# Kernel optimization log

Measured on AMD Instinct MI355X. Metric: run time of the kernel, lower is better.

## Reference

```python
import jax, jax.numpy as jnp
import numpy as np

EPS = 1e-5
ND, NDIS, NP, NG, NPW = 40000, 40000, 80000, 80000, 40000
D = 128


def gcn(x_src, src, dst, n_dst, W, b):
    # DGL GraphConv with norm='both': D_dst^{-1/2} A^T D_src^{-1/2} X W + b
    deg_out = jnp.maximum(jnp.zeros((x_src.shape[0],), x_src.dtype).at[src].add(1.0), 1.0)
    xs = x_src * (deg_out ** -0.5)[:, None]
    msg = jax.ops.segment_sum(xs[src], dst, num_segments=n_dst)
    deg_in = jnp.maximum(jnp.zeros((n_dst,), x_src.dtype).at[dst].add(1.0), 1.0)
    return (msg * (deg_in ** -0.5)[:, None]) @ W + b


def bn_prelu(v, gamma, beta, a):
    # BatchNorm1d (training-mode batch stats, biased var) then PReLU (scalar slope)
    mu = v.mean(0)
    var = v.var(0)
    y = gamma * (v - mu) / jnp.sqrt(var + EPS) + beta
    return jnp.where(y >= 0, y, a * y)


def sem_att(z, W1, b1, w2):
    # z: [N, K, D]; shared SemanticAttention across node types
    s = jnp.tanh(z @ W1 + b1) @ w2        # [N, K]
    beta = jax.nn.softmax(s.mean(0))       # [K]
    return jnp.einsum('k,nkd->nd', beta, z)


def setup_inputs():
    key = jax.random.key(0)
    ks = iter(jax.random.split(key, 40))
    f = lambda n: jax.random.normal(next(ks), (n, D), jnp.float32)
    inp = {'h_drug': f(ND), 'h_disease': f(NDIS), 'h_protein': f(NP),
           'h_gene': f(NG), 'h_pathway': f(NPW)}
    rels = {'dd': (ND, ND, 640000), 'ddi': (ND, NDIS, 640000), 'disdis': (NDIS, NDIS, 640000),
            'dp': (ND, NP, 640000), 'pp': (NP, NP, 1280000), 'pg': (NP, NG, 1280000),
            'gg': (NG, NG, 1280000), 'gpw': (NG, NPW, 1280000), 'pwpw': (NPW, NPW, 640000),
            'pwdis': (NPW, NDIS, 640000)}
    for name, (ns, nd, E) in rels.items():
        inp[name + '_src'] = jax.random.randint(next(ks), (E,), 0, ns)
        inp[name + '_dst'] = jax.random.randint(next(ks), (E,), 0, nd)
    inp['W_blocks'] = jax.random.normal(next(ks), (5, 3, D, D), jnp.float32) * 0.09
    inp['b_blocks'] = jnp.zeros((5, 3, D), jnp.float32)
    inp['bn_gamma'] = jnp.ones((5, D), jnp.float32)
    inp['bn_beta'] = jnp.zeros((5, D), jnp.float32)
    inp['prelu_a'] = jnp.full((5,), 0.25, jnp.float32)
    inp['attn_W1'] = jax.random.normal(next(ks), (D, D), jnp.float32) * 0.09
    inp['attn_b1'] = jnp.zeros((D,), jnp.float32)
    inp['attn_w2'] = jax.random.normal(next(ks), (D,), jnp.float32) * 0.09
    return inp


def reference(h_drug, h_disease, h_protein, h_gene, h_pathway,
              dd_src, dd_dst, ddi_src, ddi_dst, disdis_src, disdis_dst,
              dp_src, dp_dst, pp_src, pp_dst, pg_src, pg_dst,
              gg_src, gg_dst, gpw_src, gpw_dst, pwpw_src, pwpw_dst,
              pwdis_src, pwdis_dst,
              W_blocks, b_blocks, bn_gamma, bn_beta, prelu_a,
              attn_W1, attn_b1, attn_w2):
    act = lambda i, v: bn_prelu(v, bn_gamma[i], bn_beta[i], prelu_a[i])
    # block 0: drug_disease  (rels: drug_drug, drug_disease, disease_disease)
    d0 = act(0, gcn(h_drug, dd_src, dd_dst, ND, W_blocks[0, 0], b_blocks[0, 0]))
    dis0 = act(0, gcn(h_drug, ddi_src, ddi_dst, NDIS, W_blocks[0, 1], b_blocks[0, 1])
               + gcn(h_disease, disdis_src, disdis_dst, NDIS, W_blocks[0, 2], b_blocks[0, 2]))
    # block 1: drug_protein
    d1 = act(1, gcn(h_drug, dd_src, dd_dst, ND, W_blocks[1, 0], b_blocks[1, 0]))
    p1 = act(1, gcn(h_drug, dp_src, dp_dst, NP, W_blocks[1, 1], b_blocks[1, 1])
             + gcn(h_protein, pp_src, pp_dst, NP, W_blocks[1, 2], b_blocks[1, 2]))
    # block 2: protein_gene
    p2 = act(2, gcn(h_protein, pp_src, pp_dst, NP, W_blocks[2, 0], b_blocks[2, 0]))
    g2 = act(2, gcn(h_protein, pg_src, pg_dst, NG, W_blocks[2, 1], b_blocks[2, 1])
             + gcn(h_gene, gg_src, gg_dst, NG, W_blocks[2, 2], b_blocks[2, 2]))
    # block 3: gene_pathway
    g3 = act(3, gcn(h_gene, gg_src, gg_dst, NG, W_blocks[3, 0], b_blocks[3, 0]))
    pw3 = act(3, gcn(h_gene, gpw_src, gpw_dst, NPW, W_blocks[3, 1], b_blocks[3, 1])
              + gcn(h_pathway, pwpw_src, pwpw_dst, NPW, W_blocks[3, 2], b_blocks[3, 2]))
    # block 4: pathway_disease
    pw4 = act(4, gcn(h_pathway, pwpw_src, pwpw_dst, NPW, W_blocks[4, 0], b_blocks[4, 0]))
    dis4 = act(4, gcn(h_pathway, pwdis_src, pwdis_dst, NDIS, W_blocks[4, 1], b_blocks[4, 1])
               + gcn(h_disease, disdis_src, disdis_dst, NDIS, W_blocks[4, 2], b_blocks[4, 2]))
    att = lambda a, b: sem_att(jnp.stack([a, b], axis=1), attn_W1, attn_b1, attn_w2)
    return (att(d0, d1), att(dis0, dis4), att(p1, p2), att(g2, g3), att(pw3, pw4))
```

## Files before the change

kernel.cpp:

```cpp
#include <hip/hip_runtime.h>
#include <hip/hip_bf16.h>

#define D128 128

typedef __attribute__((ext_vector_type(8))) short bf16x8;
typedef __attribute__((ext_vector_type(4))) float f32x4;

__device__ inline unsigned short f2bf(float f) {
    unsigned u = __float_as_uint(f);
    u = u + 0x7fffu + ((u >> 16) & 1u);
    return (unsigned short)(u >> 16);
}
__device__ inline float bf2f(unsigned short h) {
    return __uint_as_float(((unsigned)h) << 16);
}
__device__ inline float fast_tanh(float x) {
    float e = __expf(2.f * x);
    return 1.f - 2.f * __builtin_amdgcn_rcpf(e + 1.f);
}

__device__ __forceinline__ void stage_w(const unsigned short* __restrict__ Wt,
                                        unsigned short* lw, int t)
{
    const uint4* srcW = (const uint4*)Wt;
    uint4* dstW = (uint4*)lw;
    for (int i = t; i < 2048; i += 256) {
        int row = i >> 4, sl = i & 15;
        dstW[row * 16 + (sl ^ (row & 7))] = srcW[i];
    }
}
__device__ __forceinline__ bf16x8 read_w(const unsigned short* lw, int row, int kt, int lq)
{
    int slot = (kt * 4 + lq) ^ (row & 7);
    return *(const bf16x8*)(lw + row * 128 + slot * 8);
}

__global__ __launch_bounds__(256) void xconv(const float* __restrict__ in,
                                             unsigned* __restrict__ out, int n_u)
{
    int i = blockIdx.x * 256 + threadIdx.x;
    if (i * 4 >= n_u) return;
    const float4* in4 = (const float4*)(in + (size_t)i * 8);
    float4 a = in4[0], b = in4[1];
    uint4 o;
    o.x = (unsigned)f2bf(a.x) | ((unsigned)f2bf(a.y) << 16);
    o.y = (unsigned)f2bf(a.z) | ((unsigned)f2bf(a.w) << 16);
    o.z = (unsigned)f2bf(b.x) | ((unsigned)f2bf(b.y) << 16);
    o.w = (unsigned)f2bf(b.z) | ((unsigned)f2bf(b.w) << 16);
    ((uint4*)out)[i] = o;
}

__global__ void wconv_t(const float* __restrict__ W_blocks, const float* __restrict__ W1,
                        unsigned short* __restrict__ wt)
{
    int m = blockIdx.x;
    const float* src = (m < 15) ? (W_blocks + (size_t)m * 16384) : W1;
    unsigned short* dst = wt + (size_t)m * 16384;
    for (int i = threadIdx.x; i < 16384; i += 256) {
        int n = i >> 7, k = i & 127;
        dst[i] = f2bf(src[k * 128 + n]);
    }
}

struct BuildArgs {
    const int* esrc[10]; const int* edst[10];
    int* histD; int* histS;
    int cumBlk[11]; int dstColBase[11]; int srcColBase[11]; int E[10];
};

__global__ __launch_bounds__(256) void part_count(BuildArgs A)
{
    __shared__ int hd[640], hs[640];
    int blk = blockIdx.x, t = threadIdx.x;
    int r = 0;
    while (r < 9 && blk >= A.cumBlk[r + 1]) r++;
    int blkInRel = blk - A.cumBlk[r];
    int nbD = A.dstColBase[r + 1] - A.dstColBase[r];
    int nbS = A.srcColBase[r + 1] - A.srcColBase[r];
    for (int i = t; i < nbD; i += 256) hd[i] = 0;
    for (int i = t; i < nbS; i += 256) hs[i] = 0;
    __syncthreads();
    int e0 = blkInRel * 4096;
    const int* sp = A.esrc[r];
    const int* dp = A.edst[r];
    int E = A.E[r];
#pragma unroll
    for (int j = 0; j < 16; j++) {
        int e = e0 + j * 256 + t;
        if (e < E) {
            atomicAdd(&hd[dp[e] >> 7], 1);
            atomicAdd(&hs[sp[e] >> 7], 1);
        }
    }
    __syncthreads();
    int cd = A.dstColBase[r], cs = A.srcColBase[r];
    for (int i = t; i < nbD; i += 256)
        A.histD[(size_t)(cd + i) * 313 + blkInRel] = hd[i];
    for (int i = t; i < nbS; i += 256)
        A.histS[(size_t)(cs + i) * 313 + blkInRel] = hs[i];
}

struct ScanArgs { int* hist; int* totals; int colBase[11]; int cumBlk[11]; };

__global__ __launch_bounds__(256) void col_scan(ScanArgs A)
{
    __shared__ int v[320];
    int col = blockIdx.x, t = threadIdx.x;
    int r = 0;
    while (r < 9 && col >= A.colBase[r + 1]) r++;
    int nblk = A.cumBlk[r + 1] - A.cumBlk[r];
    for (int i = t; i < nblk; i += 256) v[i] = A.hist[(size_t)col * 313 + i];
    __syncthreads();
    if (t == 0) {
        int run = 0;
        for (int i = 0; i < nblk; i++) { int c = v[i]; v[i] = run; run += c; }
        A.totals[col] = run;
    }
    __syncthreads();
    for (int i = t; i < nblk; i += 256) A.hist[(size_t)col * 313 + i] = v[i];
}

__global__ __launch_bounds__(256) void base_scan(const int* __restrict__ totals,
                                                 int* __restrict__ colbase, int n)
{
    __shared__ int v[4384];
    int t = threadIdx.x;
    for (int i = t; i < n; i += 256) v[i] = totals[i];
    __syncthreads();
    if (t == 0) {
        int run = 0;
        for (int i = 0; i < n; i++) { int c = v[i]; v[i] = run; run += c; }
        v[n] = run;
    }
    __syncthreads();
    for (int i = t; i <= n; i += 256) colbase[i] = v[i];
}

struct ScatArgs {
    const int* esrc[10]; const int* edst[10];
    const int* hist; const int* colbase; int* epart;
    int cumBlk[11]; int colBase[11]; int E[10];
};

__global__ __launch_bounds__(256) void part_scatter(ScatArgs A)
{
    __shared__ int h[640];
    __shared__ int base[640];
    int blk = blockIdx.x, t = threadIdx.x;
    int r = 0;
    while (r < 9 && blk >= A.cumBlk[r + 1]) r++;
    int blkInRel = blk - A.cumBlk[r];
    int colb = A.colBase[r];
    int nb = A.colBase[r + 1] - colb;
    for (int i = t; i < nb; i += 256) {
        base[i] = A.colbase[colb + i] + A.hist[(size_t)(colb + i) * 313 + blkInRel];
        h[i] = 0;
    }
    __syncthreads();
    int e0 = blkInRel * 4096;
    const int* sp = A.esrc[r];
    const int* dp = A.edst[r];
    int E = A.E[r];
#pragma unroll
    for (int j = 0; j < 16; j++) {
        int e = e0 + j * 256 + t;
        if (e < E) {
            int d = dp[e];
            int b = d >> 7;
            int p = atomicAdd(&h[b], 1);
            A.epart[base[b] + p] = (sp[e] & 0x1FFFF) | ((d & 127) << 17);
        }
    }
}

struct SScatArgs {
    const int* esrc[10];
    const int* hist; const int* colbase; unsigned char* spart;
    int cumBlk[11]; int colBase[11]; int E[10];
};

__global__ __launch_bounds__(256) void scatter_src(SScatArgs A)
{
    __shared__ int h[640];
    __shared__ int base[640];
    int blk = blockIdx.x, t = threadIdx.x;
    int r = 0;
    while (r < 9 && blk >= A.cumBlk[r + 1]) r++;
    int blkInRel = blk - A.cumBlk[r];
    int colb = A.colBase[r];
    int nb = A.colBase[r + 1] - colb;
    for (int i = t; i < nb; i += 256) {
        base[i] = A.colbase[colb + i] + A.hist[(size_t)(colb + i) * 313 + blkInRel];
        h[i] = 0;
    }
    __syncthreads();
    int e0 = blkInRel * 4096;
    const int* sp = A.esrc[r];
    int E = A.E[r];
#pragma unroll
    for (int j = 0; j < 16; j++) {
        int e = e0 + j * 256 + t;
        if (e < E) {
            int s = sp[e];
            int b = s >> 7;
            int p = atomicAdd(&h[b], 1);
            A.spart[(size_t)base[b] + p] = (unsigned char)(s & 127);
        }
    }
}

struct FillArgs {
    const int* epart; const int* colbase;
    int* cursor; int* ebuf; int* oflow;
    int colBase[11];
    int cursorBase[10]; int ebufBase[10]; int cap[10]; int nd[10];
};

__global__ __launch_bounds__(256) void bucket_fill(FillArgs A)
{
    __shared__ int lcur[128];
    int col = blockIdx.x, t = threadIdx.x;
    int r = 0;
    while (r < 9 && col >= A.colBase[r + 1]) r++;
    int b = col - A.colBase[r];
    if (t < 128) lcur[t] = 0;
    __syncthreads();
    int start = A.colbase[col], end = A.colbase[col + 1];
    int cap = A.cap[r];
    int* eb = A.ebuf + (size_t)A.ebufBase[r];
    int* ofl = A.oflow + r * 8194;
    for (int i = start + t; i < end; i += 256) {
        int v = A.epart[i];
        int s = v & 0x1FFFF;
        int dlow = (v >> 17) & 127;
        int p = atomicAdd(&lcur[dlow], 1);
        if (p < cap) eb[(size_t)(b * 128 + dlow) * cap + p] = s;
        else {
            int q = atomicAdd(&ofl[0], 1);
            if (q < 4095) { ofl[2 + 2 * q] = b * 128 + dlow; ofl[3 + 2 * q] = s; }
        }
    }
    __syncthreads();
    if (t < 128) {
        int d = b * 128 + t;
        if (d < A.nd[r]) A.cursor[A.cursorBase[r] + d] = lcur[t];
    }
}

struct DegArgs {
    const unsigned char* spart; const int* colbase;
    int* degs;
    int colBase[11]; int degsBase[10]; int ns[10];
};

__global__ __launch_bounds__(256) void deg_count(DegArgs A)
{
    __shared__ int lc[128];
    int col = blockIdx.x, t = threadIdx.x;
    int r = 0;
    while (r < 9 && col >= A.colBase[r + 1]) r++;
    int b = col - A.colBase[r];
    if (t < 128) lc[t] = 0;
    __syncthreads();
    int start = A.colbase[col], end = A.colbase[col + 1];
    for (int i = start + t; i < end; i += 256)
        atomicAdd(&lc[A.spart[i]], 1);
    __syncthreads();
    if (t < 128) {
        int s = b * 128 + t;
        if (s < A.ns[r]) A.degs[A.degsBase[r] + s] = lc[t];
    }
}

__global__ __launch_bounds__(256) void gather_bf16(
    const unsigned* __restrict__ Xb, const int* __restrict__ degs,
    const int* __restrict__ cursor, const int* __restrict__ ebuf,
    const int* __restrict__ oflow, unsigned* __restrict__ aggb, int nd, int cap)
{
    int t = threadIdx.x;
    int lane = t & 63, r = t >> 6;
    int d = blockIdx.x * 4 + r;
    if (d >= nd) return;
    int cnt = cursor[d];
    int end = min(cnt, cap);
    const int* eb = ebuf + (size_t)d * cap;
    float a0 = 0.f, a1 = 0.f;
    int i = 0;
    for (; i + 4 <= end; i += 4) {
        int s0 = eb[i], s1 = eb[i + 1], s2 = eb[i + 2], s3 = eb[i + 3];
        float c0 = rsqrtf((float)max(degs[s0], 1));
        float c1 = rsqrtf((float)max(degs[s1], 1));
        float c2 = rsqrtf((float)max(degs[s2], 1));
        float c3 = rsqrtf((float)max(degs[s3], 1));
        unsigned x0 = Xb[(size_t)s0 * 64 + lane];
        unsigned x1 = Xb[(size_t)s1 * 64 + lane];
        unsigned x2 = Xb[(size_t)s2 * 64 + lane];
        unsigned x3 = Xb[(size_t)s3 * 64 + lane];
        a0 = fmaf(bf2f((unsigned short)(x0 & 0xffff)), c0, a0);
        a1 = fmaf(bf2f((unsigned short)(x0 >> 16)), c0, a1);
        a0 = fmaf(bf2f((unsigned short)(x1 & 0xffff)), c1, a0);
        a1 = fmaf(bf2f((unsigned short)(x1 >> 16)), c1, a1);
        a0 = fmaf(bf2f((unsigned short)(x2 & 0xffff)), c2, a0);
        a1 = fmaf(bf2f((unsigned short)(x2 >> 16)), c2, a1);
        a0 = fmaf(bf2f((unsigned short)(x3 & 0xffff)), c3, a0);
        a1 = fmaf(bf2f((unsigned short)(x3 >> 16)), c3, a1);
    }
    for (; i < end; i++) {
        int s0 = eb[i];
        float c0 = rsqrtf((float)max(degs[s0], 1));
        unsigned x0 = Xb[(size_t)s0 * 64 + lane];
        a0 = fmaf(bf2f((unsigned short)(x0 & 0xffff)), c0, a0);
        a1 = fmaf(bf2f((unsigned short)(x0 >> 16)), c0, a1);
    }
    if (cnt > cap) {
        int n = min(oflow[0], 4095);
        for (int ii = 0; ii < n; ii++) {
            if (oflow[2 + 2 * ii] == d) {
                int s0 = oflow[3 + 2 * ii];
                float c0 = rsqrtf((float)max(degs[s0], 1));
                unsigned x0 = Xb[(size_t)s0 * 64 + lane];
                a0 = fmaf(bf2f((unsigned short)(x0 & 0xffff)), c0, a0);
                a1 = fmaf(bf2f((unsigned short)(x0 >> 16)), c0, a1);
            }
        }
    }
    float sc = rsqrtf((float)max(cnt, 1));
    a0 *= sc; a1 *= sc;
    aggb[(size_t)d * 64 + lane] = (unsigned)f2bf(a0) | ((unsigned)f2bf(a1) << 16);
}

__device__ __forceinline__ void epi_store(
    f32x4* acc, unsigned short* __restrict__ Vb, int accum, int do_stats,
    float* ssum, float* ssq, int row0, int lr, int lq)
{
#pragma unroll
    for (int n = 0; n < 8; n++) {
        int col = n * 16 + lr;
        float s_ = 0.f, q_ = 0.f;
#pragma unroll
        for (int reg = 0; reg < 4; reg++) {
            int row = row0 + lq * 4 + reg;
            float v = acc[n][reg];
            unsigned short* vp = &Vb[(size_t)row * D128 + col];
            if (accum) v += bf2f(*vp);
            *vp = f2bf(v);
            s_ += v; q_ += v * v;
        }
        if (do_stats) {
            s_ += __shfl_xor(s_, 16); s_ += __shfl_xor(s_, 32);
            q_ += __shfl_xor(q_, 16); q_ += __shfl_xor(q_, 32);
            if (lq == 0) {
                atomicAdd(&ssum[col], s_);
                atomicAdd(&ssq[col], q_);
            }
        }
    }
}

__global__ __launch_bounds__(256) void gemm_mfma(
    const unsigned short* __restrict__ A, const unsigned short* __restrict__ Wt,
    unsigned short* __restrict__ Vb, int accum, int do_stats, float* __restrict__ statsraw)
{
    __shared__ unsigned short lw[16384];
    __shared__ float ssum[128], ssq[128];
    int t = threadIdx.x;
    int wave = t >> 6, lane = t & 63;
    int lr = lane & 15, lq = lane >> 4;
    int row0 = blockIdx.x * 64 + wave * 16;

    if (t < 128) { ssum[t] = 0.f; ssq[t] = 0.f; }
    stage_w(Wt, lw, t);
    __syncthreads();

    f32x4 acc[8];
#pragma unroll
    for (int n = 0; n < 8; n++) acc[n] = (f32x4)(0.f);

    const unsigned short* arow = A + (size_t)(row0 + lr) * 128 + lq * 8;
#pragma unroll
    for (int kt = 0; kt < 4; kt++) {
        bf16x8 af = *(const bf16x8*)(arow + kt * 32);
#pragma unroll
        for (int n = 0; n < 8; n++) {
            bf16x8 bfr = read_w(lw, n * 16 + lr, kt, lq);
            acc[n] = __builtin_amdgcn_mfma_f32_16x16x32_bf16(af, bfr, acc[n], 0, 0, 0);
        }
    }
    epi_store(acc, Vb, accum, do_stats, ssum, ssq, row0, lr, lq);
    if (do_stats) {
        __syncthreads();
        if (t < 128) atomicAdd(&statsraw[t], ssum[t]);
        else atomicAdd(&statsraw[t], ssq[t - 128]);
    }
}

__global__ __launch_bounds__(256) void gemm_mfma2(
    const unsigned short* __restrict__ A,
    const unsigned short* __restrict__ Wt0, const unsigned short* __restrict__ Wt1,
    unsigned short* __restrict__ V0b, unsigned short* __restrict__ V1b,
    int acc0f, int acc1f, int st0, int st1,
    float* __restrict__ sr0, float* __restrict__ sr1)
{
    __shared__ unsigned short lw0[16384], lw1[16384];
    __shared__ float ssum0[128], ssq0[128], ssum1[128], ssq1[128];
    int t = threadIdx.x;
    int wave = t >> 6, lane = t & 63;
    int lr = lane & 15, lq = lane >> 4;
    int row0 = blockIdx.x * 64 + wave * 16;

    if (t < 128) { ssum0[t] = 0.f; ssq0[t] = 0.f; ssum1[t] = 0.f; ssq1[t] = 0.f; }
    stage_w(Wt0, lw0, t);
    stage_w(Wt1, lw1, t);
    __syncthreads();

    f32x4 acc0[8], acc1[8];
#pragma unroll
    for (int n = 0; n < 8; n++) { acc0[n] = (f32x4)(0.f); acc1[n] = (f32x4)(0.f); }

    const unsigned short* arow = A + (size_t)(row0 + lr) * 128 + lq * 8;
#pragma unroll
    for (int kt = 0; kt < 4; kt++) {
        bf16x8 af = *(const bf16x8*)(arow + kt * 32);
#pragma unroll
        for (int n = 0; n < 8; n++) {
            int row = n * 16 + lr;
            bf16x8 b0 = read_w(lw0, row, kt, lq);
            bf16x8 b1 = read_w(lw1, row, kt, lq);
            acc0[n] = __builtin_amdgcn_mfma_f32_16x16x32_bf16(af, b0, acc0[n], 0, 0, 0);
            acc1[n] = __builtin_amdgcn_mfma_f32_16x16x32_bf16(af, b1, acc1[n], 0, 0, 0);
        }
    }
    epi_store(acc0, V0b, acc0f, st0, ssum0, ssq0, row0, lr, lq);
    epi_store(acc1, V1b, acc1f, st1, ssum1, ssq1, row0, lr, lq);
    __syncthreads();
    if (st0) {
        if (t < 128) atomicAdd(&sr0[t], ssum0[t]);
        else atomicAdd(&sr0[t], ssq0[t - 128]);
    }
    if (st1) {
        if (t < 128) atomicAdd(&sr1[t], ssum1[t]);
        else atomicAdd(&sr1[t], ssq1[t - 128]);
    }
}

struct FinArgs { int Ms[10]; };

__global__ void bn_finalize(const float* __restrict__ raw, float* __restrict__ fin, FinArgs fa)
{
    int tt = blockIdx.x;
    int c = threadIdx.x;
    float m = (float)fa.Ms[tt];
    float s = raw[tt * 256 + c], sq = raw[tt * 256 + 128 + c];
    float mu = s / m;
    float var = fmaxf(sq / m - mu * mu, 0.f);
    fin[tt * 256 + c] = mu;
    fin[tt * 256 + 128 + c] = rsqrtf(var + 1e-5f);
}

__global__ __launch_bounds__(256) void attn_t(
    const unsigned short* __restrict__ Vb, const float* __restrict__ raw, float Minv,
    const float* __restrict__ gam, const float* __restrict__ bet,
    const float* __restrict__ pa,
    const unsigned short* __restrict__ W1t, const float* __restrict__ b1,
    const float* __restrict__ w2, float* __restrict__ Sout)
{
    __shared__ float st[256];
    __shared__ float red[4];
    int t = threadIdx.x;
    if (t < 128) {
        float mu = raw[t] * Minv;
        float var = fmaxf(raw[128 + t] * Minv - mu * mu, 0.f);
        st[t] = mu;
        st[128 + t] = rsqrtf(var + 1e-5f);
    }
    __syncthreads();

    int wave = t >> 6, lane = t & 63;
    int lr = lane & 15, lq = lane >> 4;
    int row0 = blockIdx.x * 64 + wave * 16;
    float a = *pa;

    f32x4 acc[8];
#pragma unroll
    for (int n = 0; n < 8; n++) acc[n] = (f32x4)(0.f);

    const unsigned short* vrow = Vb + (size_t)(row0 + lr) * D128;
#pragma unroll
    for (int kt = 0; kt < 4; kt++) {
        int k0 = kt * 32 + lq * 8;
        bf16x8 vv = *(const bf16x8*)(vrow + k0);
        bf16x8 af;
#pragma unroll
        for (int jj = 0; jj < 8; jj++) {
            int cc = k0 + jj;
            float y = bf2f((unsigned short)vv[jj]);
            float yy = gam[cc] * (y - st[cc]) * st[128 + cc] + bet[cc];
            yy = yy >= 0.f ? yy : a * yy;
            af[jj] = (short)f2bf(yy);
        }
#pragma unroll
        for (int n = 0; n < 8; n++) {
            bf16x8 bfr = *(const bf16x8*)(W1t + (size_t)(n * 16 + lr) * 128 + k0);
            acc[n] = __builtin_amdgcn_mfma_f32_16x16x32_bf16(af, bfr, acc[n], 0, 0, 0);
        }
    }

    float thr = 0.f;
#pragma unroll
    for (int n = 0; n < 8; n++) {
        int col = n * 16 + lr;
        float bc = b1[col], wc = w2[col];
#pragma unroll
        for (int reg = 0; reg < 4; reg++)
            thr += fast_tanh(acc[n][reg] + bc) * wc;
    }
#pragma unroll
    for (int off = 1; off < 64; off <<= 1)
        thr += __shfl_xor(thr, off);
    if (lane == 0) red[wave] = thr;
    __syncthreads();
    if (t == 0) atomicAdd(Sout, red[0] + red[1] + red[2] + red[3]);
}

struct CombArgs {
    float* outp[5]; const unsigned short* va[5]; const unsigned short* vb[5];
    const float* stats; const float* gam; const float* bet; const float* pa; const float* S;
    int ta[5]; int tb[5]; int blka[5]; int blkb[5]; float invM[5]; int cum[6];
};

__global__ void combine_all(CombArgs D)
{
    int b = blockIdx.x, t = threadIdx.x;
    int p = 0;
    while (p < 4 && b >= D.cum[p + 1]) p++;
    size_t idx = (size_t)(b - D.cum[p]) * 256 + t;
    int c = (int)(idx & 127);
    float s0 = D.S[2 * p] * D.invM[p], s1 = D.S[2 * p + 1] * D.invM[p];
    float mx = fmaxf(s0, s1);
    float e0 = expf(s0 - mx), e1 = expf(s1 - mx);
    float inv = 1.f / (e0 + e1);
    float b0 = e0 * inv, b1w = e1 * inv;
    const float* sta = D.stats + D.ta[p] * 256;
    const float* stb = D.stats + D.tb[p] * 256;
    const float* ga = D.gam + D.blka[p] * 128;
    const float* ba = D.bet + D.blka[p] * 128;
    const float* gb = D.gam + D.blkb[p] * 128;
    const float* bb = D.bet + D.blkb[p] * 128;
    float aa = D.pa[D.blka[p]], ab = D.pa[D.blkb[p]];
    float va = bf2f(D.va[p][idx]);
    float vb = bf2f(D.vb[p][idx]);
    float ya = ga[c] * (va - sta[c]) * sta[128 + c] + ba[c];
    ya = ya >= 0.f ? ya : aa * ya;
    float yb = gb[c] * (vb - stb[c]) * stb[128 + c] + bb[c];
    yb = yb >= 0.f ? yb : ab * yb;
    D.outp[p][idx] = b0 * ya + b1w * yb;
}

extern "C" void kernel_launch(void* const* d_in, const int* in_sizes, int n_in,
                              void* d_out, int out_size, void* d_ws, size_t ws_size,
                              hipStream_t stream)
{
    const float* feats[5] = {
        (const float*)d_in[0], (const float*)d_in[1], (const float*)d_in[2],
        (const float*)d_in[3], (const float*)d_in[4]
    };
    const int featN[5] = {40000, 40000, 80000, 80000, 40000};
    const float* W_blocks = (const float*)d_in[25];
    const float* bn_gamma = (const float*)d_in[27];
    const float* bn_beta  = (const float*)d_in[28];
    const float* prelu_a  = (const float*)d_in[29];
    const float* attn_W1  = (const float*)d_in[30];
    const float* attn_b1  = (const float*)d_in[31];
    const float* attn_w2  = (const float*)d_in[32];
    float* out = (float*)d_out;

    unsigned* xbf  = (unsigned*)out;
    unsigned* aggb = (unsigned*)(out + 5120000);
    int*      ebuf = (int*)(out + 10240000);

    float* wsf = (float*)d_ws;
    unsigned short* wsvb = (unsigned short*)wsf;
    unsigned short* wtbf = (unsigned short*)(wsf + 35840000);
    int* degs     = (int*)(wsf + 35971072);
    int* cursor   = degs + 560000;
    int* oflow    = cursor + 560000;
    int* histD    = oflow + 81940;
    int* histS    = histD + 1370314;
    int* colbaseD = histS + 1370314;
    int* totalsD  = colbaseD + 4379;
    int* colbaseS = totalsD + 4378;
    int* totalsS  = colbaseS + 4379;
    int* epart    = totalsS + 4378;
    unsigned char* spart = (unsigned char*)(epart + 8960000);
    float* statsraw = (float*)(epart + 8960000 + 2240000);
    float* statsfin = statsraw + 2560;
    float* Ssum     = statsfin + 2560;
    size_t needed = ((size_t)((float*)(Ssum + 16) - wsf)) * 4;
    if (ws_size < needed) return;

    const int Mt[10]  = {40000, 40000, 40000, 40000, 80000, 80000, 80000, 80000, 40000, 40000};
    const int blk[10] = {0, 1, 0, 4, 1, 2, 2, 3, 3, 4};
    size_t offV[10];
    {
        size_t o = 0;
        for (int t = 0; t < 10; t++) { offV[t] = o; o += (size_t)Mt[t] * 128; }
    }
    unsigned short* Vb[10];
    for (int t = 0; t < 10; t++) Vb[t] = wsvb + offV[t];
    const size_t offT[5] = {0, 5120000, 10240000, 20480000, 30720000};

    const int relFeat[10] = {0, 0, 0, 1, 2, 2, 3, 3, 4, 4};
    const int relSrc[10]  = {5, 7, 11, 9, 13, 15, 17, 19, 21, 23};
    const int relNs[10]   = {40000, 40000, 40000, 40000, 80000, 80000, 80000, 80000, 40000, 40000};
    const int relNd[10]   = {40000, 40000, 80000, 40000, 80000, 80000, 80000, 40000, 40000, 40000};
    const int relE[10]    = {640000, 640000, 640000, 640000, 1280000,
                             1280000, 1280000, 1280000, 640000, 640000};
    const int relCap[10]  = {40, 40, 24, 40, 40, 40, 40, 56, 40, 40};
    const int cumBlk[11]  = {0, 157, 314, 471, 628, 941, 1254, 1567, 1880, 2037, 2194};
    const int dstColBase[11] = {0, 313, 626, 1251, 1564, 2189, 2814, 3439, 3752, 4065, 4378};
    const int srcColBase[11] = {0, 313, 626, 939, 1252, 1877, 2502, 3127, 3752, 4065, 4378};
    const int degsBase[10]   = {0, 40000, 80000, 120000, 160000, 240000, 320000, 400000, 480000, 520000};
    const int cursorBase[10] = {0, 40000, 80000, 160000, 200000, 280000, 360000, 440000, 480000, 520000};
    const int ebufBase[10]   = {0, 1600000, 3200000, 5120000, 6720000, 9920000,
                                13120000, 16320000, 18560000, 20160000};

    struct GJob { int tid; int widx; int accum; int stats; };
    const int relNjob[10] = {2, 1, 1, 2, 2, 1, 2, 1, 2, 1};
    const GJob relJob[10][2] = {
        {{0,  0, 0, 1}, {1,  3, 0, 1}},
        {{2,  1, 0, 0}, {0,  0, 0, 0}},
        {{4,  4, 0, 0}, {0,  0, 0, 0}},
        {{2,  2, 1, 1}, {3, 14, 0, 0}},
        {{4,  5, 1, 1}, {5,  6, 0, 1}},
        {{6,  7, 0, 0}, {0,  0, 0, 0}},
        {{6,  8, 1, 1}, {7,  9, 0, 1}},
        {{8, 10, 0, 0}, {0,  0, 0, 0}},
        {{8, 11, 1, 1}, {9, 12, 0, 1}},
        {{3, 13, 1, 1}, {0,  0, 0, 0}},
    };
    const int doneCnt[10] = {2, 0, 0, 1, 2, 0, 2, 0, 2, 1};
    const int doneT[10][2] = {{0,1},{0,0},{0,0},{2,0},{4,5},{0,0},{6,7},{0,0},{8,9},{3,0}};

    wconv_t<<<16, 256, 0, stream>>>(W_blocks, attn_W1, wtbf);
    hipMemsetAsync(statsraw, 0, (2560 + 2560 + 16) * sizeof(float), stream);
    hipMemsetAsync(oflow, 0, (size_t)81940 * sizeof(int), stream);

    BuildArgs BA;
    ScanArgs  SAD, SAS;
    ScatArgs  CA;
    SScatArgs SSA;
    FillArgs  FA;
    DegArgs   DA;
    for (int r = 0; r < 10; r++) {
        BA.esrc[r] = (const int*)d_in[relSrc[r]];
        BA.edst[r] = (const int*)d_in[relSrc[r] + 1];
        BA.E[r] = relE[r];
        CA.esrc[r] = BA.esrc[r]; CA.edst[r] = BA.edst[r]; CA.E[r] = relE[r];
        SSA.esrc[r] = BA.esrc[r]; SSA.E[r] = relE[r];
        FA.cursorBase[r] = cursorBase[r];
        FA.ebufBase[r] = ebufBase[r];
        FA.cap[r] = relCap[r];
        FA.nd[r] = relNd[r];
        DA.degsBase[r] = degsBase[r];
        DA.ns[r] = relNs[r];
    }
    for (int i = 0; i < 11; i++) {
        BA.cumBlk[i] = cumBlk[i]; BA.dstColBase[i] = dstColBase[i]; BA.srcColBase[i] = srcColBase[i];
        SAD.colBase[i] = dstColBase[i]; SAD.cumBlk[i] = cumBlk[i];
        SAS.colBase[i] = srcColBase[i]; SAS.cumBlk[i] = cumBlk[i];
        CA.cumBlk[i] = cumBlk[i]; CA.colBase[i] = dstColBase[i];
        SSA.cumBlk[i] = cumBlk[i]; SSA.colBase[i] = srcColBase[i];
        FA.colBase[i] = dstColBase[i];
        DA.colBase[i] = srcColBase[i];
    }
    BA.histD = histD; BA.histS = histS;
    SAD.hist = histD; SAD.totals = totalsD;
    SAS.hist = histS; SAS.totals = totalsS;
    CA.hist = histD; CA.colbase = colbaseD; CA.epart = epart;
    SSA.hist = histS; SSA.colbase = colbaseS; SSA.spart = spart;
    FA.epart = epart; FA.colbase = colbaseD;
    FA.cursor = cursor; FA.ebuf = ebuf; FA.oflow = oflow;
    DA.spart = spart; DA.colbase = colbaseS; DA.degs = degs;

    part_count<<<2194, 256, 0, stream>>>(BA);
    col_scan<<<4378, 256, 0, stream>>>(SAD);
    col_scan<<<4378, 256, 0, stream>>>(SAS);
    base_scan<<<1, 256, 0, stream>>>(totalsD, colbaseD, 4378);
    base_scan<<<1, 256, 0, stream>>>(totalsS, colbaseS, 4378);
    part_scatter<<<2194, 256, 0, stream>>>(CA);
    scatter_src<<<2194, 256, 0, stream>>>(SSA);
    bucket_fill<<<4378, 256, 0, stream>>>(FA);
    deg_count<<<4378, 256, 0, stream>>>(DA);

    int lastFeat = -1;
    for (int r = 0; r < 10; r++) {
        if (relFeat[r] != lastFeat) {
            lastFeat = relFeat[r];
            int n_u = featN[lastFeat] * 64;
            xconv<<<(n_u / 4 + 255) / 256, 256, 0, stream>>>(feats[lastFeat], xbf, n_u);
        }
        gather_bf16<<<relNd[r] / 4, 256, 0, stream>>>(
            xbf, degs + degsBase[r], cursor + cursorBase[r],
            ebuf + (size_t)ebufBase[r], oflow + r * 8194, aggb, relNd[r], relCap[r]);
        if (relNjob[r] == 2) {
            const GJob& G0 = relJob[r][0];
            const GJob& G1 = relJob[r][1];
            gemm_mfma2<<<relNd[r] / 64, 256, 0, stream>>>(
                (const unsigned short*)aggb,
                wtbf + (size_t)G0.widx * 16384, wtbf + (size_t)G1.widx * 16384,
                Vb[G0.tid], Vb[G1.tid], G0.accum, G1.accum, G0.stats, G1.stats,
                statsraw + (size_t)G0.tid * 256, statsraw + (size_t)G1.tid * 256);
        } else {
            const GJob& G = relJob[r][0];
            gemm_mfma<<<relNd[r] / 64, 256, 0, stream>>>(
                (const unsigned short*)aggb, wtbf + (size_t)G.widx * 16384,
                Vb[G.tid], G.accum, G.stats, statsraw + (size_t)G.tid * 256);
        }
        for (int k = 0; k < doneCnt[r]; k++) {
            int t = doneT[r][k];
            attn_t<<<Mt[t] / 64, 256, 0, stream>>>(
                Vb[t], statsraw + (size_t)t * 256, 1.0f / Mt[t],
                bn_gamma + blk[t] * 128, bn_beta + blk[t] * 128, prelu_a + blk[t],
                wtbf + (size_t)15 * 16384, attn_b1, attn_w2, Ssum + t);
        }
    }

    FinArgs fa;
    for (int t = 0; t < 10; t++) fa.Ms[t] = Mt[t];
    bn_finalize<<<10, 128, 0, stream>>>(statsraw, statsfin, fa);

    CombArgs CD;
    CD.stats = statsfin; CD.gam = bn_gamma; CD.bet = bn_beta; CD.pa = prelu_a; CD.S = Ssum;
    CD.cum[0] = 0;
    for (int p = 0; p < 5; p++) {
        CD.outp[p] = out + offT[p];
        CD.va[p] = Vb[p * 2];
        CD.vb[p] = Vb[p * 2 + 1];
        CD.ta[p] = p * 2; CD.tb[p] = p * 2 + 1;
        CD.blka[p] = blk[p * 2]; CD.blkb[p] = blk[p * 2 + 1];
        CD.invM[p] = 1.0f / Mt[p * 2];
        CD.cum[p + 1] = CD.cum[p] + Mt[p * 2] / 2;
    }
    combine_all<<<CD.cum[5], 256, 0, stream>>>(CD);
}
```

Before: 1.673 ms.

## Prescale source features by degree, widen partition buckets, fuse scatter kernels

The bf16 feature conversion now folds the source-degree rsqrt scale into the converted rows, so the gather no longer reads degs per edge or does a multiply per neighbour. Partition buckets grow from 128 to 512 destination rows and 256 source rows, which shrinks the histogram, scan and fill grids. The separate dst and src scatter passes are merged into one kernel that reads each edge once. In exchange, the conversion runs once per relation instead of once per feature change, and the larger buckets put more LDS atomic contention on each block.

Measured after the change: 1.617 ms. 1.03x faster.

```diff
diff --git a/kernel.cpp b/kernel.cpp
--- a/kernel.cpp
+++ b/kernel.cpp
@@ -35,19 +35,18 @@
     return *(const bf16x8*)(lw + row * 128 + slot * 8);
 }
 
-__global__ __launch_bounds__(256) void xconv(const float* __restrict__ in,
-                                             unsigned* __restrict__ out, int n_u)
-{
-    int i = blockIdx.x * 256 + threadIdx.x;
-    if (i * 4 >= n_u) return;
-    const float4* in4 = (const float4*)(in + (size_t)i * 8);
-    float4 a = in4[0], b = in4[1];
-    uint4 o;
-    o.x = (unsigned)f2bf(a.x) | ((unsigned)f2bf(a.y) << 16);
-    o.y = (unsigned)f2bf(a.z) | ((unsigned)f2bf(a.w) << 16);
-    o.z = (unsigned)f2bf(b.x) | ((unsigned)f2bf(b.y) << 16);
-    o.w = (unsigned)f2bf(b.z) | ((unsigned)f2bf(b.w) << 16);
-    ((uint4*)out)[i] = o;
+__global__ __launch_bounds__(256) void xconv_scaled(
+    const float* __restrict__ in, const int* __restrict__ degs,
+    unsigned* __restrict__ out, int nrows)
+{
+    int t = threadIdx.x;
+    int lane = t & 63, rr = t >> 6;
+    int row = blockIdx.x * 4 + rr;
+    if (row >= nrows) return;
+    float sc = rsqrtf((float)max(degs[row], 1));
+    float2 v = ((const float2*)(in + (size_t)row * 128))[lane];
+    out[(size_t)row * 64 + lane] =
+        (unsigned)f2bf(v.x * sc) | ((unsigned)f2bf(v.y * sc) << 16);
 }
 
 __global__ void wconv_t(const float* __restrict__ W_blocks, const float* __restrict__ W1,
@@ -70,7 +69,7 @@
 
 __global__ __launch_bounds__(256) void part_count(BuildArgs A)
 {
-    __shared__ int hd[640], hs[640];
+    __shared__ int hd[160], hs[320];
     int blk = blockIdx.x, t = threadIdx.x;
     int r = 0;
     while (r < 9 && blk >= A.cumBlk[r + 1]) r++;
@@ -88,8 +87,8 @@
     for (int j = 0; j < 16; j++) {
         int e = e0 + j * 256 + t;
         if (e < E) {
-            atomicAdd(&hd[dp[e] >> 7], 1);
-            atomicAdd(&hs[sp[e] >> 7], 1);
+            atomicAdd(&hd[dp[e] >> 9], 1);
+            atomicAdd(&hs[sp[e] >> 8], 1);
         }
     }
     __syncthreads();
@@ -123,7 +122,7 @@
 __global__ __launch_bounds__(256) void base_scan(const int* __restrict__ totals,
                                                  int* __restrict__ colbase, int n)
 {
-    __shared__ int v[4384];
+    __shared__ int v[2200];
     int t = threadIdx.x;
     for (int i = t; i < n; i += 256) v[i] = totals[i];
     __syncthreads();
@@ -138,23 +137,29 @@
 
 struct ScatArgs {
     const int* esrc[10]; const int* edst[10];
-    const int* hist; const int* colbase; int* epart;
-    int cumBlk[11]; int colBase[11]; int E[10];
+    const int* histD; const int* colbaseD;
+    const int* histS; const int* colbaseS;
+    int* epart; unsigned char* spart;
+    int cumBlk[11]; int dstColBase[11]; int srcColBase[11]; int E[10];
 };
 
-__global__ __launch_bounds__(256) void part_scatter(ScatArgs A)
-{
-    __shared__ int h[640];
-    __shared__ int base[640];
+__global__ __launch_bounds__(256) void scatter_all(ScatArgs A)
+{
+    __shared__ int hd[160], based[160], hs[320], bases[320];
     int blk = blockIdx.x, t = threadIdx.x;
     int r = 0;
     while (r < 9 && blk >= A.cumBlk[r + 1]) r++;
     int blkInRel = blk - A.cumBlk[r];
-    int colb = A.colBase[r];
-    int nb = A.colBase[r + 1] - colb;
-    for (int i = t; i < nb; i += 256) {
-        base[i] = A.colbase[colb + i] + A.hist[(size_t)(colb + i) * 313 + blkInRel];
-        h[i] = 0;
+    int cd = A.dstColBase[r], cs = A.srcColBase[r];
+    int nbD = A.dstColBase[r + 1] - cd;
+    int nbS = A.srcColBase[r + 1] - cs;
+    for (int i = t; i < nbD; i += 256) {
+        based[i] = A.colbaseD[cd + i] + A.histD[(size_t)(cd + i) * 313 + blkInRel];
+        hd[i] = 0;
+    }
+    for (int i = t; i < nbS; i += 256) {
+        bases[i] = A.colbaseS[cs + i] + A.histS[(size_t)(cs + i) * 313 + blkInRel];
+        hs[i] = 0;
     }
     __syncthreads();
     int e0 = blkInRel * 4096;
@@ -165,46 +170,13 @@
     for (int j = 0; j < 16; j++) {
         int e = e0 + j * 256 + t;
         if (e < E) {
-            int d = dp[e];
-            int b = d >> 7;
-            int p = atomicAdd(&h[b], 1);
-            A.epart[base[b] + p] = (sp[e] & 0x1FFFF) | ((d & 127) << 17);
-        }
-    }
-}
-
-struct SScatArgs {
-    const int* esrc[10];
-    const int* hist; const int* colbase; unsigned char* spart;
-    int cumBlk[11]; int colBase[11]; int E[10];
-};
-
-__global__ __launch_bounds__(256) void scatter_src(SScatArgs A)
-{
-    __shared__ int h[640];
-    __shared__ int base[640];
-    int blk = blockIdx.x, t = threadIdx.x;
-    int r = 0;
-    while (r < 9 && blk >= A.cumBlk[r + 1]) r++;
-    int blkInRel = blk - A.cumBlk[r];
-    int colb = A.colBase[r];
-    int nb = A.colBase[r + 1] - colb;
-    for (int i = t; i < nb; i += 256) {
-        base[i] = A.colbase[colb + i] + A.hist[(size_t)(colb + i) * 313 + blkInRel];
-        h[i] = 0;
-    }
-    __syncthreads();
-    int e0 = blkInRel * 4096;
-    const int* sp = A.esrc[r];
-    int E = A.E[r];
-#pragma unroll
-    for (int j = 0; j < 16; j++) {
-        int e = e0 + j * 256 + t;
-        if (e < E) {
-            int s = sp[e];
-            int b = s >> 7;
-            int p = atomicAdd(&h[b], 1);
-            A.spart[(size_t)base[b] + p] = (unsigned char)(s & 127);
+            int s = sp[e], d = dp[e];
+            int bd = d >> 9;
+            int pd = atomicAdd(&hd[bd], 1);
+            A.epart[based[bd] + pd] = (s & 0x1FFFF) | ((d & 511) << 17);
+            int bs = s >> 8;
+            int ps = atomicAdd(&hs[bs], 1);
+            A.spart[(size_t)bases[bs] + ps] = (unsigned char)(s & 255);
         }
     }
 }
@@ -218,12 +190,12 @@
 
 __global__ __launch_bounds__(256) void bucket_fill(FillArgs A)
 {
-    __shared__ int lcur[128];
+    __shared__ int lcur[512];
     int col = blockIdx.x, t = threadIdx.x;
     int r = 0;
     while (r < 9 && col >= A.colBase[r + 1]) r++;
     int b = col - A.colBase[r];
-    if (t < 128) lcur[t] = 0;
+    for (int i = t; i < 512; i += 256) lcur[i] = 0;
     __syncthreads();
     int start = A.colbase[col], end = A.colbase[col + 1];
     int cap = A.cap[r];
@@ -232,18 +204,18 @@
     for (int i = start + t; i < end; i += 256) {
         int v = A.epart[i];
         int s = v & 0x1FFFF;
-        int dlow = (v >> 17) & 127;
+        int dlow = (v >> 17) & 511;
         int p = atomicAdd(&lcur[dlow], 1);
-        if (p < cap) eb[(size_t)(b * 128 + dlow) * cap + p] = s;
+        if (p < cap) eb[(size_t)(b * 512 + dlow) * cap + p] = s;
         else {
             int q = atomicAdd(&ofl[0], 1);
-            if (q < 4095) { ofl[2 + 2 * q] = b * 128 + dlow; ofl[3 + 2 * q] = s; }
-        }
-    }
-    __syncthreads();
-    if (t < 128) {
-        int d = b * 128 + t;
-        if (d < A.nd[r]) A.cursor[A.cursorBase[r] + d] = lcur[t];
+            if (q < 4095) { ofl[2 + 2 * q] = b * 512 + dlow; ofl[3 + 2 * q] = s; }
+        }
+    }
+    __syncthreads();
+    for (int i = t; i < 512; i += 256) {
+        int d = b * 512 + i;
+        if (d < A.nd[r]) A.cursor[A.cursorBase[r] + d] = lcur[i];
     }
 }
 
@@ -255,25 +227,23 @@
 
 __global__ __launch_bounds__(256) void deg_count(DegArgs A)
 {
-    __shared__ int lc[128];
+    __shared__ int lc[256];
     int col = blockIdx.x, t = threadIdx.x;
     int r = 0;
     while (r < 9 && col >= A.colBase[r + 1]) r++;
     int b = col - A.colBase[r];
-    if (t < 128) lc[t] = 0;
+    lc[t] = 0;
     __syncthreads();
     int start = A.colbase[col], end = A.colbase[col + 1];
     for (int i = start + t; i < end; i += 256)
         atomicAdd(&lc[A.spart[i]], 1);
     __syncthreads();
-    if (t < 128) {
-        int s = b * 128 + t;
-        if (s < A.ns[r]) A.degs[A.degsBase[r] + s] = lc[t];
-    }
+    int s = b * 256 + t;
+    if (s < A.ns[r]) A.degs[A.degsBase[r] + s] = lc[t];
 }
 
 __global__ __launch_bounds__(256) void gather_bf16(
-    const unsigned* __restrict__ Xb, const int* __restrict__ degs,
+    const unsigned* __restrict__ Xb,
     const int* __restrict__ cursor, const int* __restrict__ ebuf,
     const int* __restrict__ oflow, unsigned* __restrict__ aggb, int nd, int cap)
 {
@@ -288,39 +258,29 @@
     int i = 0;
     for (; i + 4 <= end; i += 4) {
         int s0 = eb[i], s1 = eb[i + 1], s2 = eb[i + 2], s3 = eb[i + 3];
-        float c0 = rsqrtf((float)max(degs[s0], 1));
-        float c1 = rsqrtf((float)max(degs[s1], 1));
-        float c2 = rsqrtf((float)max(degs[s2], 1));
-        float c3 = rsqrtf((float)max(degs[s3], 1));
         unsigned x0 = Xb[(size_t)s0 * 64 + lane];
         unsigned x1 = Xb[(size_t)s1 * 64 + lane];
         unsigned x2 = Xb[(size_t)s2 * 64 + lane];
         unsigned x3 = Xb[(size_t)s3 * 64 + lane];
-        a0 = fmaf(bf2f((unsigned short)(x0 & 0xffff)), c0, a0);
-        a1 = fmaf(bf2f((unsigned short)(x0 >> 16)), c0, a1);
-        a0 = fmaf(bf2f((unsigned short)(x1 & 0xffff)), c1, a0);
-        a1 = fmaf(bf2f((unsigned short)(x1 >> 16)), c1, a1);
-        a0 = fmaf(bf2f((unsigned short)(x2 & 0xffff)), c2, a0);
-        a1 = fmaf(bf2f((unsigned short)(x2 >> 16)), c2, a1);
-        a0 = fmaf(bf2f((unsigned short)(x3 & 0xffff)), c3, a0);
-        a1 = fmaf(bf2f((unsigned short)(x3 >> 16)), c3, a1);
+        a0 += bf2f((unsigned short)(x0 & 0xffff)) + bf2f((unsigned short)(x1 & 0xffff))
+            + bf2f((unsigned short)(x2 & 0xffff)) + bf2f((unsigned short)(x3 & 0xffff));
+        a1 += bf2f((unsigned short)(x0 >> 16)) + bf2f((unsigned short)(x1 >> 16))
+            + bf2f((unsigned short)(x2 >> 16)) + bf2f((unsigned short)(x3 >> 16));
     }
     for (; i < end; i++) {
         int s0 = eb[i];
-        float c0 = rsqrtf((float)max(degs[s0], 1));
         unsigned x0 = Xb[(size_t)s0 * 64 + lane];
-        a0 = fmaf(bf2f((unsigned short)(x0 & 0xffff)), c0, a0);
-        a1 = fmaf(bf2f((unsigned short)(x0 >> 16)), c0, a1);
+        a0 += bf2f((unsigned short)(x0 & 0xffff));
+        a1 += bf2f((unsigned short)(x0 >> 16));
     }
     if (cnt > cap) {
         int n = min(oflow[0], 4095);
         for (int ii = 0; ii < n; ii++) {
             if (oflow[2 + 2 * ii] == d) {
                 int s0 = oflow[3 + 2 * ii];
-                float c0 = rsqrtf((float)max(degs[s0], 1));
                 unsigned x0 = Xb[(size_t)s0 * 64 + lane];
-                a0 = fmaf(bf2f((unsigned short)(x0 & 0xffff)), c0, a0);
-                a1 = fmaf(bf2f((unsigned short)(x0 >> 16)), c0, a1);
+                a0 += bf2f((unsigned short)(x0 & 0xffff));
+                a1 += bf2f((unsigned short)(x0 >> 16));
             }
         }
     }
@@ -585,12 +545,12 @@
     int* cursor   = degs + 560000;
     int* oflow    = cursor + 560000;
     int* histD    = oflow + 81940;
-    int* histS    = histD + 1370314;
-    int* colbaseD = histS + 1370314;
-    int* totalsD  = colbaseD + 4379;
-    int* colbaseS = totalsD + 4378;
-    int* totalsS  = colbaseS + 4379;
-    int* epart    = totalsS + 4378;
+    int* histS    = histD + 344926;
+    int* colbaseD = histS + 686722;
+    int* totalsD  = colbaseD + 1103;
+    int* colbaseS = totalsD + 1102;
+    int* totalsS  = colbaseS + 2195;
+    int* epart    = totalsS + 2194;
     unsigned char* spart = (unsigned char*)(epart + 8960000);
     float* statsraw = (float*)(epart + 8960000 + 2240000);
     float* statsfin = statsraw + 2560;
@@ -617,8 +577,8 @@
                              1280000, 1280000, 1280000, 640000, 640000};
     const int relCap[10]  = {40, 40, 24, 40, 40, 40, 40, 56, 40, 40};
     const int cumBlk[11]  = {0, 157, 314, 471, 628, 941, 1254, 1567, 1880, 2037, 2194};
-    const int dstColBase[11] = {0, 313, 626, 1251, 1564, 2189, 2814, 3439, 3752, 4065, 4378};
-    const int srcColBase[11] = {0, 313, 626, 939, 1252, 1877, 2502, 3127, 3752, 4065, 4378};
+    const int dstColBase[11] = {0, 79, 158, 315, 394, 551, 708, 865, 944, 1023, 1102};
+    const int srcColBase[11] = {0, 157, 314, 471, 628, 941, 1254, 1567, 1880, 2037, 2194};
     const int degsBase[10]   = {0, 40000, 80000, 120000, 160000, 240000, 320000, 400000, 480000, 520000};
     const int cursorBase[10] = {0, 40000, 80000, 160000, 200000, 280000, 360000, 440000, 480000, 520000};
     const int ebufBase[10]   = {0, 1600000, 3200000, 5120000, 6720000, 9920000,
@@ -648,7 +608,6 @@
     BuildArgs BA;
     ScanArgs  SAD, SAS;
     ScatArgs  CA;
-    SScatArgs SSA;
     FillArgs  FA;
     DegArgs   DA;
     for (int r = 0; r < 10; r++) {
@@ -656,7 +615,6 @@
         BA.edst[r] = (const int*)d_in[relSrc[r] + 1];
         BA.E[r] = relE[r];
         CA.esrc[r] = BA.esrc[r]; CA.edst[r] = BA.edst[r]; CA.E[r] = relE[r];
-        SSA.esrc[r] = BA.esrc[r]; SSA.E[r] = relE[r];
         FA.cursorBase[r] = cursorBase[r];
         FA.ebufBase[r] = ebufBase[r];
         FA.cap[r] = relCap[r];
@@ -668,39 +626,34 @@
         BA.cumBlk[i] = cumBlk[i]; BA.dstColBase[i] = dstColBase[i]; BA.srcColBase[i] = srcColBase[i];
         SAD.colBase[i] = dstColBase[i]; SAD.cumBlk[i] = cumBlk[i];
         SAS.colBase[i] = srcColBase[i]; SAS.cumBlk[i] = cumBlk[i];
-        CA.cumBlk[i] = cumBlk[i]; CA.colBase[i] = dstColBase[i];
-        SSA.cumBlk[i] = cumBlk[i]; SSA.colBase[i] = srcColBase[i];
+        CA.cumBlk[i] = cumBlk[i]; CA.dstColBase[i] = dstColBase[i]; CA.srcColBase[i] = srcColBase[i];
         FA.colBase[i] = dstColBase[i];
         DA.colBase[i] = srcColBase[i];
     }
     BA.histD = histD; BA.histS = histS;
     SAD.hist = histD; SAD.totals = totalsD;
     SAS.hist = histS; SAS.totals = totalsS;
-    CA.hist = histD; CA.colbase = colbaseD; CA.epart = epart;
-    SSA.hist = histS; SSA.colbase = colbaseS; SSA.spart = spart;
+    CA.histD = histD; CA.colbaseD = colbaseD;
+    CA.histS = histS; CA.colbaseS = colbaseS;
+    CA.epart = epart; CA.spart = spart;
     FA.epart = epart; FA.colbase = colbaseD;
     FA.cursor = cursor; FA.ebuf = ebuf; FA.oflow = oflow;
     DA.spart = spart; DA.colbase = colbaseS; DA.degs = degs;
 
     part_count<<<2194, 256, 0, stream>>>(BA);
-    col_scan<<<4378, 256, 0, stream>>>(SAD);
-    col_scan<<<4378, 256, 0, stream>>>(SAS);
-    base_scan<<<1, 256, 0, stream>>>(totalsD, colbaseD, 4378);
-    base_scan<<<1, 256, 0, stream>>>(totalsS, colbaseS, 4378);
-    part_scatter<<<2194, 256, 0, stream>>>(CA);
-    scatter_src<<<2194, 256, 0, stream>>>(SSA);
-    bucket_fill<<<4378, 256, 0, stream>>>(FA);
-    deg_count<<<4378, 256, 0, stream>>>(DA);
-
-    int lastFeat = -1;
+    col_scan<<<1102, 256, 0, stream>>>(SAD);
+    col_scan<<<2194, 256, 0, stream>>>(SAS);
+    base_scan<<<1, 256, 0, stream>>>(totalsD, colbaseD, 1102);
+    base_scan<<<1, 256, 0, stream>>>(totalsS, colbaseS, 2194);
+    scatter_all<<<2194, 256, 0, stream>>>(CA);
+    bucket_fill<<<1102, 256, 0, stream>>>(FA);
+    deg_count<<<2194, 256, 0, stream>>>(DA);
+
     for (int r = 0; r < 10; r++) {
-        if (relFeat[r] != lastFeat) {
-            lastFeat = relFeat[r];
-            int n_u = featN[lastFeat] * 64;
-            xconv<<<(n_u / 4 + 255) / 256, 256, 0, stream>>>(feats[lastFeat], xbf, n_u);
-        }
+        xconv_scaled<<<(relNs[r] + 3) / 4, 256, 0, stream>>>(
+            feats[relFeat[r]], degs + degsBase[r], xbf, relNs[r]);
         gather_bf16<<<relNd[r] / 4, 256, 0, stream>>>(
-            xbf, degs + degsBase[r], cursor + cursorBase[r],
+            xbf, cursor + cursorBase[r],
             ebuf + (size_t)ebufBase[r], oflow + r * 8194, aggb, relNd[r], relCap[r]);
         if (relNjob[r] == 2) {
             const GJob& G0 = relJob[r][0];
```
